# Performance work log

Measured on AMD Instinct MI355X. Metric: run time of the kernel, lower is better.

The kernel has to match this reference:

```python
import jax, jax.numpy as jnp
import numpy as np

VOCAB = 50257
H = 1024
T = 4096


def setup_inputs() -> dict:
    key = jax.random.key(0)
    ks = jax.random.split(key, 6)
    scale = 1.0 / np.sqrt(H)  # matches torch LSTM uniform(-1/sqrt(H), 1/sqrt(H)) scale
    return {
        "tokens": jax.random.randint(ks[0], (T,), 0, VOCAB),
        "emb": jax.random.normal(ks[1], (VOCAB, H), dtype=jnp.float32) * 0.02,
        "w_ih": jax.random.uniform(ks[2], (4 * H, H), jnp.float32, -scale, scale),
        "w_hh": jax.random.uniform(ks[3], (4 * H, H), jnp.float32, -scale, scale),
        "b_ih": jax.random.uniform(ks[4], (4 * H,), jnp.float32, -scale, scale),
        "b_hh": jax.random.uniform(ks[5], (4 * H,), jnp.float32, -scale, scale),
    }


def _lstm(x, w_ih, w_hh, b_ih, b_hh):
    # x: [T, H]. Precompute input-side gate projections for all timesteps.
    gx = x @ w_ih.T + (b_ih + b_hh)  # [T, 4H]

    def step(carry, g_t):
        h, c = carry  # [H], [H]
        gates = g_t + h @ w_hh.T  # [4H]
        i, f, g, o = jnp.split(gates, 4)  # torch gate order: input, forget, cell, output
        i = jax.nn.sigmoid(i)
        f = jax.nn.sigmoid(f)
        g = jnp.tanh(g)
        o = jax.nn.sigmoid(o)
        c = f * c + i * g
        h = o * jnp.tanh(c)
        return (h, c), h

    h0 = jnp.zeros((H,), x.dtype)
    c0 = jnp.zeros((H,), x.dtype)
    (h_f, c_f), hs = jax.lax.scan(step, (h0, c0), gx)
    return hs, h_f, c_f  # hs: [T, H]


def reference(tokens, emb, w_ih, w_hh, b_ih, b_hh):
    x = emb[tokens]  # [T, H] embedding lookup
    hs, h_f, c_f = _lstm(x, w_ih, w_hh, b_ih, b_hh)
    output = hs[None, :, :]          # [1, T, H]  (batch_first, batch=1)
    h_n = h_f[None, None, :]         # [1, 1, H]
    c_n = c_f[None, None, :]         # [1, 1, H]
    return (output, (h_n, c_n))
```

## Files before the change

### kernel.cpp

```cpp
#include <hip/hip_runtime.h>
#include <hip/hip_bf16.h>

#define HD   1024
#define GD   4096
#define TT   4096
#define NWG  256

__global__ void embed_kernel(const int* __restrict__ tokens,
                             const float* __restrict__ emb,
                             float* __restrict__ X) {
    int t = blockIdx.x;
    int tok = tokens[t];
    const float4* src = reinterpret_cast<const float4*>(emb + (size_t)tok * HD);
    float4* dst = reinterpret_cast<float4*>(X + (size_t)t * HD);
    dst[threadIdx.x] = src[threadIdx.x];
}

#define BM 128
#define BN 128
#define BK 16
#define LDP 132

__global__ __launch_bounds__(256, 2) void gemm_gx(
    const float* __restrict__ X,
    const float* __restrict__ Wih,
    const float* __restrict__ bih,
    const float* __restrict__ bhh,
    float* __restrict__ gxout)
{
    __shared__ float As[BK][LDP];
    __shared__ float Bs[BK][LDP];
    const int tid = threadIdx.x;
    const int m0 = blockIdx.x * BM;
    const int n0 = blockIdx.y * BN;
    const int tx = tid & 15;
    const int ty = tid >> 4;

    float acc[8][8] = {};

    for (int kt = 0; kt < HD; kt += BK) {
#pragma unroll
        for (int p = 0; p < 2; ++p) {
            int e = p * 256 + tid;
            int row = e >> 2;
            int quad = e & 3;
            float4 av = *reinterpret_cast<const float4*>(
                &X[(size_t)(m0 + row) * HD + kt + quad * 4]);
            float4 bv = *reinterpret_cast<const float4*>(
                &Wih[(size_t)(n0 + row) * HD + kt + quad * 4]);
            As[quad * 4 + 0][row] = av.x;
            As[quad * 4 + 1][row] = av.y;
            As[quad * 4 + 2][row] = av.z;
            As[quad * 4 + 3][row] = av.w;
            Bs[quad * 4 + 0][row] = bv.x;
            Bs[quad * 4 + 1][row] = bv.y;
            Bs[quad * 4 + 2][row] = bv.z;
            Bs[quad * 4 + 3][row] = bv.w;
        }
        __syncthreads();
#pragma unroll
        for (int k = 0; k < BK; ++k) {
            float4 a0 = *reinterpret_cast<const float4*>(&As[k][ty * 8]);
            float4 a1 = *reinterpret_cast<const float4*>(&As[k][ty * 8 + 4]);
            float4 b0 = *reinterpret_cast<const float4*>(&Bs[k][tx * 8]);
            float4 b1 = *reinterpret_cast<const float4*>(&Bs[k][tx * 8 + 4]);
            float a[8] = {a0.x, a0.y, a0.z, a0.w, a1.x, a1.y, a1.z, a1.w};
            float b[8] = {b0.x, b0.y, b0.z, b0.w, b1.x, b1.y, b1.z, b1.w};
#pragma unroll
            for (int i = 0; i < 8; ++i)
#pragma unroll
                for (int j = 0; j < 8; ++j)
                    acc[i][j] += a[i] * b[j];
        }
        __syncthreads();
    }

    float bias[8];
#pragma unroll
    for (int j = 0; j < 8; ++j) {
        int n = n0 + tx * 8 + j;
        bias[j] = bih[n] + bhh[n];
    }
#pragma unroll
    for (int i = 0; i < 8; ++i) {
        size_t o = (size_t)(m0 + ty * 8 + i) * GD + n0 + tx * 8;
        float4 s0 = {acc[i][0] + bias[0], acc[i][1] + bias[1],
                     acc[i][2] + bias[2], acc[i][3] + bias[3]};
        float4 s1 = {acc[i][4] + bias[4], acc[i][5] + bias[5],
                     acc[i][6] + bias[6], acc[i][7] + bias[7]};
        *reinterpret_cast<float4*>(&gxout[o]) = s0;
        *reinterpret_cast<float4*>(&gxout[o + 4]) = s1;
    }
}

__global__ __launch_bounds__(256, 1) void lstm_scan(
    const float* __restrict__ gx,
    const float* __restrict__ whh,
    float* __restrict__ out,
    unsigned long long* __restrict__ hbuf)
{
    const int tid = threadIdx.x;
    const int b = blockIdx.x;
    const int chunk = tid & 15;
    const int row_local = tid >> 4;
    const int gate = row_local >> 2;
    const int jj = row_local & 3;
    const int R = gate * HD + b * 4 + jj;

    float w[64];
    {
        const float4* wp = reinterpret_cast<const float4*>(
            whh + (size_t)R * HD + chunk * 64);
#pragma unroll
        for (int q = 0; q < 16; ++q) {
            float4 v = wp[q];
            w[q * 4 + 0] = v.x; w[q * 4 + 1] = v.y;
            w[q * 4 + 2] = v.z; w[q * 4 + 3] = v.w;
        }
    }

    __shared__ float h_lds[HD];
    __shared__ float gsum[16];

#pragma unroll
    for (int q = 0; q < 4; ++q) h_lds[tid * 4 + q] = 0.f;
    __syncthreads();

    const bool leader = (tid < 4);
    const int j_out = b * 4 + tid;
    float c_reg = 0.f;

    float gxi = 0.f, gxf = 0.f, gxg = 0.f, gxo = 0.f;
    if (leader) {
        const float* gr = gx;
        gxi = gr[j_out];
        gxf = gr[HD + j_out];
        gxg = gr[2 * HD + j_out];
        gxo = gr[3 * HD + j_out];
    }

    for (int step = 1; step <= TT; ++step) {
        float ni = 0.f, nf = 0.f, ng = 0.f, no = 0.f;
        if (leader && step < TT) {
            const float* gr = gx + (size_t)step * GD;
            ni = gr[j_out];
            nf = gr[HD + j_out];
            ng = gr[2 * HD + j_out];
            no = gr[3 * HD + j_out];
        }

        float acc = 0.f;
        {
            const float4* hb4 = reinterpret_cast<const float4*>(&h_lds[chunk * 64]);
#pragma unroll
            for (int q = 0; q < 16; ++q) {
                float4 hv = hb4[q];
                acc += w[q * 4 + 0] * hv.x;
                acc += w[q * 4 + 1] * hv.y;
                acc += w[q * 4 + 2] * hv.z;
                acc += w[q * 4 + 3] * hv.w;
            }
        }
        acc += __shfl_xor(acc, 1, 64);
        acc += __shfl_xor(acc, 2, 64);
        acc += __shfl_xor(acc, 4, 64);
        acc += __shfl_xor(acc, 8, 64);
        if (chunk == 0) gsum[row_local] = acc;
        __syncthreads();

        if (leader) {
            float xi = gsum[0 * 4 + tid] + gxi;
            float xf = gsum[1 * 4 + tid] + gxf;
            float xg = gsum[2 * 4 + tid] + gxg;
            float xo = gsum[3 * 4 + tid] + gxo;
            float ii = 1.f / (1.f + __expf(-xi));
            float ff = 1.f / (1.f + __expf(-xf));
            float gg = tanhf(xg);
            float oo = 1.f / (1.f + __expf(-xo));
            c_reg = ff * c_reg + ii * gg;
            float hh = oo * tanhf(c_reg);

            unsigned long long pkt =
                ((unsigned long long)(unsigned)step << 32) | __float_as_uint(hh);
            __hip_atomic_store(&hbuf[(step & 1) * HD + j_out], pkt,
                               __ATOMIC_RELAXED, __HIP_MEMORY_SCOPE_AGENT);
            h_lds[j_out] = hh;
            out[(size_t)(step - 1) * HD + j_out] = hh;
            if (step == TT) {
                out[(size_t)TT * HD + j_out] = hh;
                out[(size_t)TT * HD + HD + j_out] = c_reg;
            }
            gxi = ni; gxf = nf; gxg = ng; gxo = no;
        }

        if (step < TT) {
            if (tid != b) {
                unsigned long long* src = &hbuf[(step & 1) * HD + tid * 4];
                unsigned long long v0 = 0, v1 = 0, v2 = 0, v3 = 0;
                bool k0 = false, k1 = false, k2 = false, k3 = false;
                const unsigned int tag = (unsigned int)step;
                int guard = 0;
                for (;;) {
                    if (!k0) v0 = __hip_atomic_load(&src[0], __ATOMIC_RELAXED,
                                                    __HIP_MEMORY_SCOPE_AGENT);
                    if (!k1) v1 = __hip_atomic_load(&src[1], __ATOMIC_RELAXED,
                                                    __HIP_MEMORY_SCOPE_AGENT);
                    if (!k2) v2 = __hip_atomic_load(&src[2], __ATOMIC_RELAXED,
                                                    __HIP_MEMORY_SCOPE_AGENT);
                    if (!k3) v3 = __hip_atomic_load(&src[3], __ATOMIC_RELAXED,
                                                    __HIP_MEMORY_SCOPE_AGENT);
                    k0 = k0 || ((unsigned int)(v0 >> 32) == tag);
                    k1 = k1 || ((unsigned int)(v1 >> 32) == tag);
                    k2 = k2 || ((unsigned int)(v2 >> 32) == tag);
                    k3 = k3 || ((unsigned int)(v3 >> 32) == tag);
                    if (k0 & k1 & k2 & k3) break;
                    if (++guard > (1 << 20)) break;
                    __builtin_amdgcn_s_sleep(1);
                }
                h_lds[tid * 4 + 0] = __uint_as_float((unsigned int)v0);
                h_lds[tid * 4 + 1] = __uint_as_float((unsigned int)v1);
                h_lds[tid * 4 + 2] = __uint_as_float((unsigned int)v2);
                h_lds[tid * 4 + 3] = __uint_as_float((unsigned int)v3);
            }
            __syncthreads();
        }
    }
}

extern "C" void kernel_launch(void* const* d_in, const int* in_sizes, int n_in,
                              void* d_out, int out_size, void* d_ws, size_t ws_size,
                              hipStream_t stream) {
    const int*   tokens = (const int*)d_in[0];
    const float* emb    = (const float*)d_in[1];
    const float* w_ih   = (const float*)d_in[2];
    const float* w_hh   = (const float*)d_in[3];
    const float* b_ih   = (const float*)d_in[4];
    const float* b_hh   = (const float*)d_in[5];
    float* out = (float*)d_out;

    char* ws = (char*)d_ws;
    unsigned long long* hbuf = (unsigned long long*)ws;
    float* X  = (float*)(ws + (size_t)16384);
    float* gx = (float*)(ws + (size_t)16384 + (size_t)TT * HD * 4);

    hipMemsetAsync(hbuf, 0, 2 * HD * sizeof(unsigned long long), stream);
    embed_kernel<<<TT, 256, 0, stream>>>(tokens, emb, X);
    gemm_gx<<<dim3(TT / BM, GD / BN), 256, 0, stream>>>(X, w_ih, b_ih, b_hh, gx);
    lstm_scan<<<NWG, 256, 0, stream>>>(gx, w_hh, out, hbuf);
}
```

Measured before the change: 19.82 ms.

## Map one hidden unit per wavefront to remove intra-block barrier in LSTM scan

Reorganizes the persistent LSTM scan so each wavefront owns one hidden unit with all four gate rows, reducing gate sums by shuffles instead of going through shared memory and a __syncthreads. The gx bias is folded into the accumulator, h in LDS is double-buffered, loads use a strided interleaved layout with FMA, and tanh is replaced by an exp-based formula. This removes one block barrier and the serial leader-only gate phase per timestep. In exchange every lane computes the activations redundantly, and the exp-based tanh is less accurate than tanhf.

```diff
diff --git a/kernel.cpp b/kernel.cpp
--- a/kernel.cpp
+++ b/kernel.cpp
@@ -93,112 +93,102 @@
     }
 }
 
+__device__ __forceinline__ float sigmoid_(float x) {
+    return 1.f / (1.f + __expf(-x));
+}
+__device__ __forceinline__ float tanh_(float x) {
+    return __builtin_fmaf(2.f, 1.f / (1.f + __expf(-2.f * x)), -1.f);
+}
+
 __global__ __launch_bounds__(256, 1) void lstm_scan(
     const float* __restrict__ gx,
     const float* __restrict__ whh,
     float* __restrict__ out,
     unsigned long long* __restrict__ hbuf)
 {
-    const int tid = threadIdx.x;
-    const int b = blockIdx.x;
-    const int chunk = tid & 15;
-    const int row_local = tid >> 4;
-    const int gate = row_local >> 2;
-    const int jj = row_local & 3;
-    const int R = gate * HD + b * 4 + jj;
+    const int tid   = threadIdx.x;
+    const int b     = blockIdx.x;
+    const int lane  = tid & 63;
+    const int wv    = tid >> 6;
+    const int chunk = lane & 15;
+    const int gate  = lane >> 4;
+    const int j     = b * 4 + wv;
+    const int R     = gate * HD + j;
 
     float w[64];
     {
-        const float4* wp = reinterpret_cast<const float4*>(
-            whh + (size_t)R * HD + chunk * 64);
+        const float* wrow = whh + (size_t)R * HD;
 #pragma unroll
         for (int q = 0; q < 16; ++q) {
-            float4 v = wp[q];
+            float4 v = *reinterpret_cast<const float4*>(&wrow[chunk * 4 + q * 64]);
             w[q * 4 + 0] = v.x; w[q * 4 + 1] = v.y;
             w[q * 4 + 2] = v.z; w[q * 4 + 3] = v.w;
         }
     }
 
-    __shared__ float h_lds[HD];
-    __shared__ float gsum[16];
-
-#pragma unroll
-    for (int q = 0; q < 4; ++q) h_lds[tid * 4 + q] = 0.f;
+    __shared__ float h_lds[2][HD];
+#pragma unroll
+    for (int q = 0; q < 4; ++q) h_lds[0][tid * 4 + q] = 0.f;
     __syncthreads();
 
-    const bool leader = (tid < 4);
-    const int j_out = b * 4 + tid;
     float c_reg = 0.f;
-
-    float gxi = 0.f, gxf = 0.f, gxg = 0.f, gxo = 0.f;
-    if (leader) {
-        const float* gr = gx;
-        gxi = gr[j_out];
-        gxf = gr[HD + j_out];
-        gxg = gr[2 * HD + j_out];
-        gxo = gr[3 * HD + j_out];
-    }
-
-    for (int step = 1; step <= TT; ++step) {
-        float ni = 0.f, nf = 0.f, ng = 0.f, no = 0.f;
-        if (leader && step < TT) {
-            const float* gr = gx + (size_t)step * GD;
-            ni = gr[j_out];
-            nf = gr[HD + j_out];
-            ng = gr[2 * HD + j_out];
-            no = gr[3 * HD + j_out];
-        }
-
-        float acc = 0.f;
+    float gx_cur = gx[R];
+
+    for (int s = 1; s <= TT; ++s) {
+        const int cb = (s - 1) & 1;
+        const int nb = s & 1;
+
+        float gx_nxt = 0.f;
+        if (s < TT) gx_nxt = gx[(size_t)s * GD + R];
+
+        float acc = (chunk == 0) ? gx_cur : 0.f;
         {
-            const float4* hb4 = reinterpret_cast<const float4*>(&h_lds[chunk * 64]);
+            const float* hb = h_lds[cb];
 #pragma unroll
             for (int q = 0; q < 16; ++q) {
-                float4 hv = hb4[q];
-                acc += w[q * 4 + 0] * hv.x;
-                acc += w[q * 4 + 1] * hv.y;
-                acc += w[q * 4 + 2] * hv.z;
-                acc += w[q * 4 + 3] * hv.w;
+                float4 hv = *reinterpret_cast<const float4*>(&hb[chunk * 4 + q * 64]);
+                acc = __builtin_fmaf(w[q * 4 + 0], hv.x, acc);
+                acc = __builtin_fmaf(w[q * 4 + 1], hv.y, acc);
+                acc = __builtin_fmaf(w[q * 4 + 2], hv.z, acc);
+                acc = __builtin_fmaf(w[q * 4 + 3], hv.w, acc);
             }
         }
         acc += __shfl_xor(acc, 1, 64);
         acc += __shfl_xor(acc, 2, 64);
         acc += __shfl_xor(acc, 4, 64);
         acc += __shfl_xor(acc, 8, 64);
-        if (chunk == 0) gsum[row_local] = acc;
-        __syncthreads();
-
-        if (leader) {
-            float xi = gsum[0 * 4 + tid] + gxi;
-            float xf = gsum[1 * 4 + tid] + gxf;
-            float xg = gsum[2 * 4 + tid] + gxg;
-            float xo = gsum[3 * 4 + tid] + gxo;
-            float ii = 1.f / (1.f + __expf(-xi));
-            float ff = 1.f / (1.f + __expf(-xf));
-            float gg = tanhf(xg);
-            float oo = 1.f / (1.f + __expf(-xo));
-            c_reg = ff * c_reg + ii * gg;
-            float hh = oo * tanhf(c_reg);
-
+        float si = __shfl(acc, 0, 64);
+        float sf = __shfl(acc, 16, 64);
+        float sg = __shfl(acc, 32, 64);
+        float so = __shfl(acc, 48, 64);
+
+        float ii = sigmoid_(si);
+        float ff = sigmoid_(sf);
+        float gg = tanh_(sg);
+        float oo = sigmoid_(so);
+        c_reg = __builtin_fmaf(ff, c_reg, ii * gg);
+        float hh = oo * tanh_(c_reg);
+
+        if (lane == 0) {
             unsigned long long pkt =
-                ((unsigned long long)(unsigned)step << 32) | __float_as_uint(hh);
-            __hip_atomic_store(&hbuf[(step & 1) * HD + j_out], pkt,
+                ((unsigned long long)(unsigned)s << 32) | __float_as_uint(hh);
+            __hip_atomic_store(&hbuf[(size_t)nb * HD + j], pkt,
                                __ATOMIC_RELAXED, __HIP_MEMORY_SCOPE_AGENT);
-            h_lds[j_out] = hh;
-            out[(size_t)(step - 1) * HD + j_out] = hh;
-            if (step == TT) {
-                out[(size_t)TT * HD + j_out] = hh;
-                out[(size_t)TT * HD + HD + j_out] = c_reg;
+            h_lds[nb][j] = hh;
+            out[(size_t)(s - 1) * HD + j] = hh;
+            if (s == TT) {
+                out[(size_t)TT * HD + j] = hh;
+                out[(size_t)TT * HD + HD + j] = c_reg;
             }
-            gxi = ni; gxf = nf; gxg = ng; gxo = no;
-        }
-
-        if (step < TT) {
+        }
+        gx_cur = gx_nxt;
+
+        if (s < TT) {
             if (tid != b) {
-                unsigned long long* src = &hbuf[(step & 1) * HD + tid * 4];
+                unsigned long long* src = &hbuf[(size_t)nb * HD + tid * 4];
                 unsigned long long v0 = 0, v1 = 0, v2 = 0, v3 = 0;
                 bool k0 = false, k1 = false, k2 = false, k3 = false;
-                const unsigned int tag = (unsigned int)step;
+                const unsigned int tag = (unsigned int)s;
                 int guard = 0;
                 for (;;) {
                     if (!k0) v0 = __hip_atomic_load(&src[0], __ATOMIC_RELAXED,
@@ -214,13 +204,15 @@
                     k2 = k2 || ((unsigned int)(v2 >> 32) == tag);
                     k3 = k3 || ((unsigned int)(v3 >> 32) == tag);
                     if (k0 & k1 & k2 & k3) break;
-                    if (++guard > (1 << 20)) break;
+                    if (++guard > (1 << 18)) break;
                     __builtin_amdgcn_s_sleep(1);
                 }
-                h_lds[tid * 4 + 0] = __uint_as_float((unsigned int)v0);
-                h_lds[tid * 4 + 1] = __uint_as_float((unsigned int)v1);
-                h_lds[tid * 4 + 2] = __uint_as_float((unsigned int)v2);
-                h_lds[tid * 4 + 3] = __uint_as_float((unsigned int)v3);
+                float4 hv;
+                hv.x = __uint_as_float((unsigned int)v0);
+                hv.y = __uint_as_float((unsigned int)v1);
+                hv.z = __uint_as_float((unsigned int)v2);
+                hv.w = __uint_as_float((unsigned int)v3);
+                *reinterpret_cast<float4*>(&h_lds[nb][tid * 4]) = hv;
             }
             __syncthreads();
         }
```

New measurement: 15.97 ms. 19.4% less time.
